# Kernel tuning notes

Measured on AMD Instinct MI355X. Metric: run time of the kernel, lower is better.

The kernel has to match this reference:

```python
import jax, jax.numpy as jnp
import numpy as np
from functools import partial

H = 50  # hidden size hardcoded in the module


def _lstm_cell(x, h, c, W_ih, W_hh, b_ih, b_hh):
    # PyTorch LSTMCell math, gate order i, f, g, o
    gates = x @ W_ih.T + h @ W_hh.T + b_ih + b_hh  # [B, 4H]
    i, f, g, o = jnp.split(gates, 4, axis=-1)
    c_new = jax.nn.sigmoid(f) * c + jax.nn.sigmoid(i) * jnp.tanh(g)
    h_new = jax.nn.sigmoid(o) * jnp.tanh(c_new)
    return h_new, c_new


def setup_inputs() -> dict:
    key = jax.random.key(0)
    ks = jax.random.split(key, 11)
    B, T = 512, 1024

    def w(k, shape, fan_in):
        return (jax.random.normal(k, shape, jnp.float32) / np.sqrt(fan_in)).astype(jnp.float32)

    return {
        "x": jax.random.normal(ks[0], (B, T), jnp.float32),
        "W_ih1": w(ks[1], (4 * H, 1), H),
        "W_hh1": w(ks[2], (4 * H, H), H),
        "b_ih1": w(ks[3], (4 * H,), H),
        "b_hh1": w(ks[4], (4 * H,), H),
        "W_ih2": w(ks[5], (4 * H, H), H),
        "W_hh2": w(ks[6], (4 * H, H), H),
        "b_ih2": w(ks[7], (4 * H,), H),
        "b_hh2": w(ks[8], (4 * H,), H),
        "W_lin": w(ks[9], (1, H), H),
        "b_lin": w(ks[10], (1,), H),
        "predict": 32,
    }


def reference(x, W_ih1, W_hh1, b_ih1, b_hh1, W_ih2, W_hh2, b_ih2, b_hh2,
              W_lin, b_lin, predict):
    B = x.shape[0]
    z = jnp.zeros((B, H), x.dtype)
    init = (z, z, z, z)

    def step(carry, x_t):  # x_t: [B, 1]
        h1, c1, h2, c2 = carry
        h1, c1 = _lstm_cell(x_t, h1, c1, W_ih1, W_hh1, b_ih1, b_hh1)
        h2, c2 = _lstm_cell(h1, h2, c2, W_ih2, W_hh2, b_ih2, b_hh2)
        out = h2 @ W_lin.T + b_lin  # [B, 1]
        return (h1, c1, h2, c2), out

    xs = jnp.swapaxes(x, 0, 1)[:, :, None]  # [T, B, 1]
    carry, outs = jax.lax.scan(step, init, xs)  # outs: [T, B, 1]

    if predict > 0:
        h1, c1, h2, c2 = carry

        def pstep(pcarry, _):
            h1, c1, h2, c2, o = pcarry
            h1, c1 = _lstm_cell(o, h1, c1, W_ih1, W_hh1, b_ih1, b_hh1)
            h2, c2 = _lstm_cell(h1, h2, c2, W_ih2, W_hh2, b_ih2, b_hh2)
            out = h2 @ W_lin.T + b_lin
            return (h1, c1, h2, c2, out), out

        _, pouts = jax.lax.scan(pstep, (h1, c1, h2, c2, outs[-1]), None, length=predict)
        outs = jnp.concatenate([outs, pouts], axis=0)

    # stack(dim=1).squeeze(2) -> [B, T + predict]
    return jnp.swapaxes(outs[..., 0], 0, 1)
```

## Files before the change

kernel.cpp:

```cpp
#include <hip/hip_runtime.h>


#define Hh   50
#define TLEN 1024

typedef _Float16 half2v __attribute__((ext_vector_type(2)));

#if __has_builtin(__builtin_amdgcn_fdot2)
#define FDOT2(a, b, c) __builtin_amdgcn_fdot2((a), (b), (c), false)
#else
#define FDOT2(a, b, c) ((c) + (float)(a)[0] * (float)(b)[0] + (float)(a)[1] * (float)(b)[1])
#endif

#define BC(f) __builtin_bit_cast(half2v, f)

#define DOT25(A0, A1, A2, A3, BASE, H) do {                                  \
    _Pragma("unroll")                                                        \
    for (int pq = 0; pq < 6; ++pq) {                                         \
        A0 = FDOT2(wgt[(BASE) + 4*pq + 0], BC(H[4*pq + 0]), A0);             \
        A1 = FDOT2(wgt[(BASE) + 4*pq + 1], BC(H[4*pq + 1]), A1);             \
        A2 = FDOT2(wgt[(BASE) + 4*pq + 2], BC(H[4*pq + 2]), A2);             \
        A3 = FDOT2(wgt[(BASE) + 4*pq + 3], BC(H[4*pq + 3]), A3);             \
    }                                                                        \
    A0 = FDOT2(wgt[(BASE) + 24], BC(H[24]), A0);                             \
} while (0)

__device__ __forceinline__ float fast_sigmoid(float v) {
    return 1.0f / (1.0f + __expf(-v));
}
__device__ __forceinline__ float fast_tanh(float v) {
    return 1.0f - 2.0f / (__expf(2.0f * v) + 1.0f);
}

extern "C" __global__ __launch_bounds__(256, 2)
void sine_lstm_kernel(const float* __restrict__ x,
                      const float* __restrict__ W_ih1,
                      const float* __restrict__ W_hh1,
                      const float* __restrict__ b_ih1,
                      const float* __restrict__ b_hh1,
                      const float* __restrict__ W_ih2,
                      const float* __restrict__ W_hh2,
                      const float* __restrict__ b_ih2,
                      const float* __restrict__ b_hh2,
                      const float* __restrict__ W_lin,
                      const float* __restrict__ b_lin,
                      const int*   __restrict__ predict_p,
                      float* __restrict__ out,
                      int T)
{
    __shared__ __align__(16) float    x_lds[TLEN];
    __shared__ __align__(16) _Float16 h1lds[2][64];
    __shared__ __align__(16) _Float16 h2lds[2][64];
    __shared__ __align__(16) float    h2f32[2][64];

    const int tid = threadIdx.x;
    const int wv  = tid >> 6;
    const int ln  = tid & 63;
    const bool isProd = (wv < 2);
    const int b   = blockIdx.x;
    const int predict = *predict_p;
    const int S = T + predict;

    for (int i = tid; i < TLEN; i += 256)
        x_lds[i] = x[(size_t)b * T + i];
    if (tid < 128) {
        ((_Float16*)h1lds)[tid] = (_Float16)0.0f;
        ((_Float16*)h2lds)[tid] = (_Float16)0.0f;
        ((float*)h2f32)[tid] = 0.0f;
    }

    const int  m    = (wv & 1) * 32 + (ln >> 1);
    const int  sub  = ln & 1;
    const bool mval = (m < Hh);
    const bool owner = mval && (sub == 0);
    const int  mc   = mval ? m : 0;
    const int  rowP = sub ? (Hh + mc)  : mc;
    const int  rowQ = sub ? (150 + mc) : (100 + mc);

    const float* MA = isProd ? W_hh1 : W_ih2;
    const float* MB = isProd ? W_hh1 : W_hh2;
    half2v wgt[100];
    #pragma unroll
    for (int p = 0; p < 25; ++p) {
        const int k0 = 2 * p, k1 = 2 * p + 1;
        wgt[p]      = half2v{(_Float16)MA[rowP * Hh + k0], (_Float16)MA[rowP * Hh + k1]};
        wgt[25 + p] = half2v{(_Float16)MA[rowQ * Hh + k0], (_Float16)MA[rowQ * Hh + k1]};
        wgt[50 + p] = half2v{(_Float16)MB[rowP * Hh + k0], (_Float16)MB[rowP * Hh + k1]};
        wgt[75 + p] = half2v{(_Float16)MB[rowQ * Hh + k0], (_Float16)MB[rowQ * Hh + k1]};
    }
    const float bP = isProd ? (b_ih1[rowP] + b_hh1[rowP]) : (b_ih2[rowP] + b_hh2[rowP]);
    const float bQ = isProd ? (b_ih1[rowQ] + b_hh1[rowQ]) : (b_ih2[rowQ] + b_hh2[rowQ]);
    const float wihP = W_ih1[rowP], wihQ = W_ih1[rowQ];
    const float wlin_l = (ln < Hh) ? W_lin[ln] : 0.0f;
    const float blin   = b_lin[0];

    float h1r[25], h2r[25];
    #pragma unroll
    for (int p = 0; p < 25; ++p) { h1r[p] = 0.0f; h2r[p] = 0.0f; }
    float cst = 0.0f;

    __syncthreads();

    for (int t = 0; t <= S; ++t) {
        __syncthreads();
        {
            const int s1 = (t + 1) & 1;
            #pragma unroll
            for (int L = 0; L < 6; ++L) {
                float4 f = *(const float4*)&h1lds[s1][8 * L];
                h1r[4*L] = f.x; h1r[4*L+1] = f.y; h1r[4*L+2] = f.z; h1r[4*L+3] = f.w;
            }
            h1r[24] = *(const float*)&h1lds[s1][48];
            const int s2 = t & 1;
            #pragma unroll
            for (int L = 0; L < 6; ++L) {
                float4 f = *(const float4*)&h2lds[s2][8 * L];
                h2r[4*L] = f.x; h2r[4*L+1] = f.y; h2r[4*L+2] = f.z; h2r[4*L+3] = f.w;
            }
            h2r[24] = *(const float*)&h2lds[s2][48];
        }
        const bool pred = (t >= T);

        if (!isProd && t >= 1) {
            float p0 = bP, p1 = 0.0f, p2 = 0.0f, p3 = 0.0f;
            float q0 = bQ, q1 = 0.0f, q2 = 0.0f, q3 = 0.0f;
            DOT25(p0, p1, p2, p3, 0,  h1r);
            DOT25(p0, p1, p2, p3, 50, h2r);
            DOT25(q0, q1, q2, q3, 25, h1r);
            DOT25(q0, q1, q2, q3, 75, h2r);
            float gP = (p0 + p2) + (p1 + p3);
            float gQ = (q0 + q2) + (q1 + q3);
            float eP = __shfl_xor(gP, 1);
            float eQ = __shfl_xor(gQ, 1);
            if (owner) {
                float cn = fast_sigmoid(eP) * cst + fast_sigmoid(gP) * fast_tanh(gQ);
                cst = cn;
                float hn = fast_sigmoid(eQ) * fast_tanh(cn);
                h2lds[(t + 1) & 1][m] = (_Float16)hn;
                h2f32[(t + 1) & 1][m] = hn;
            }
        }

        if (wv == 0 && t >= 2 && t <= T) {
            float part = (ln < Hh) ? h2f32[t & 1][ln] * wlin_l : 0.0f;
            #pragma unroll
            for (int off = 32; off > 0; off >>= 1)
                part += __shfl_down(part, off);
            if (ln == 0) out[(size_t)b * S + (t - 2)] = part + blin;
        }

        if (!pred) {
            if (isProd) {
                float xin = x_lds[t];
                float p0 = bP + xin * wihP, p1 = 0.0f, p2 = 0.0f, p3 = 0.0f;
                float q0 = bQ + xin * wihQ, q1 = 0.0f, q2 = 0.0f, q3 = 0.0f;
                DOT25(p0, p1, p2, p3, 0,  h1r);
                DOT25(q0, q1, q2, q3, 25, h1r);
                float gP = (p0 + p2) + (p1 + p3);
                float gQ = (q0 + q2) + (q1 + q3);
                float eP = __shfl_xor(gP, 1);
                float eQ = __shfl_xor(gQ, 1);
                if (owner) {
                    float cn = fast_sigmoid(eP) * cst + fast_sigmoid(gP) * fast_tanh(gQ);
                    cst = cn;
                    h1lds[t & 1][m] = (_Float16)(fast_sigmoid(eQ) * fast_tanh(cn));
                }
            }
        } else {
            __syncthreads();
            float part = (ln < Hh) ? h2f32[(t + 1) & 1][ln] * wlin_l : 0.0f;
            #pragma unroll
            for (int off = 32; off > 0; off >>= 1)
                part += __shfl_down(part, off);
            float o = __shfl(part, 0) + blin;
            if (tid == 0) out[(size_t)b * S + (t - 1)] = o;
            if (isProd && t < S) {
                float p0 = bP + o * wihP, p1 = 0.0f, p2 = 0.0f, p3 = 0.0f;
                float q0 = bQ + o * wihQ, q1 = 0.0f, q2 = 0.0f, q3 = 0.0f;
                DOT25(p0, p1, p2, p3, 0,  h1r);
                DOT25(q0, q1, q2, q3, 25, h1r);
                float gP = (p0 + p2) + (p1 + p3);
                float gQ = (q0 + q2) + (q1 + q3);
                float eP = __shfl_xor(gP, 1);
                float eQ = __shfl_xor(gQ, 1);
                if (owner) {
                    float cn = fast_sigmoid(eP) * cst + fast_sigmoid(gP) * fast_tanh(gQ);
                    cst = cn;
                    h1lds[t & 1][m] = (_Float16)(fast_sigmoid(eQ) * fast_tanh(cn));
                }
            }
        }
    }
}

extern "C" void kernel_launch(void* const* d_in, const int* in_sizes, int n_in,
                              void* d_out, int out_size, void* d_ws, size_t ws_size,
                              hipStream_t stream) {
    const float* x      = (const float*)d_in[0];
    const float* W_ih1  = (const float*)d_in[1];
    const float* W_hh1  = (const float*)d_in[2];
    const float* b_ih1  = (const float*)d_in[3];
    const float* b_hh1  = (const float*)d_in[4];
    const float* W_ih2  = (const float*)d_in[5];
    const float* W_hh2  = (const float*)d_in[6];
    const float* b_ih2  = (const float*)d_in[7];
    const float* b_hh2  = (const float*)d_in[8];
    const float* W_lin  = (const float*)d_in[9];
    const float* b_lin  = (const float*)d_in[10];
    const int*   pred   = (const int*)d_in[11];
    float* out = (float*)d_out;

    const int B = 512;
    const int T = in_sizes[0] / B;

    dim3 grid(B), block(256);
    hipLaunchKernelGGL(sine_lstm_kernel, grid, block, 0, stream,
                       x, W_ih1, W_hh1, b_ih1, b_hh1,
                       W_ih2, W_hh2, b_ih2, b_hh2,
                       W_lin, b_lin, pred, out, T);
}
```

Baseline: 1.064 ms.

## Split gate rows across four lanes per hidden unit with 512-thread blocks

Doubles the block to 512 threads and assigns each lane a single gate row, so four lanes cooperate per hidden unit instead of two lanes each computing two rows. This halves the per-thread dot-product chain on each serial timestep and halves the weight registers per thread. In exchange it adds a third cross-lane shuffle per step, raises the wave count per block, and puts more pressure on per-CU occupancy. Producer waves also stop loading the unused h2 state.

```diff
diff --git a/kernel.cpp b/kernel.cpp
--- a/kernel.cpp
+++ b/kernel.cpp
@@ -14,15 +14,15 @@
 
 #define BC(f) __builtin_bit_cast(half2v, f)
 
-#define DOT25(A0, A1, A2, A3, BASE, H) do {                                  \
+#define DOT25(A0, A1, A2, A3, W, H) do {                                     \
     _Pragma("unroll")                                                        \
     for (int pq = 0; pq < 6; ++pq) {                                         \
-        A0 = FDOT2(wgt[(BASE) + 4*pq + 0], BC(H[4*pq + 0]), A0);             \
-        A1 = FDOT2(wgt[(BASE) + 4*pq + 1], BC(H[4*pq + 1]), A1);             \
-        A2 = FDOT2(wgt[(BASE) + 4*pq + 2], BC(H[4*pq + 2]), A2);             \
-        A3 = FDOT2(wgt[(BASE) + 4*pq + 3], BC(H[4*pq + 3]), A3);             \
+        A0 = FDOT2(W[4*pq + 0], BC(H[4*pq + 0]), A0);                        \
+        A1 = FDOT2(W[4*pq + 1], BC(H[4*pq + 1]), A1);                        \
+        A2 = FDOT2(W[4*pq + 2], BC(H[4*pq + 2]), A2);                        \
+        A3 = FDOT2(W[4*pq + 3], BC(H[4*pq + 3]), A3);                        \
     }                                                                        \
-    A0 = FDOT2(wgt[(BASE) + 24], BC(H[24]), A0);                             \
+    A0 = FDOT2(W[24], BC(H[24]), A0);                                        \
 } while (0)
 
 __device__ __forceinline__ float fast_sigmoid(float v) {
@@ -32,7 +32,7 @@
     return 1.0f - 2.0f / (__expf(2.0f * v) + 1.0f);
 }
 
-extern "C" __global__ __launch_bounds__(256, 2)
+extern "C" __global__ __launch_bounds__(512, 2)
 void sine_lstm_kernel(const float* __restrict__ x,
                       const float* __restrict__ W_ih1,
                       const float* __restrict__ W_hh1,
@@ -56,12 +56,12 @@
     const int tid = threadIdx.x;
     const int wv  = tid >> 6;
     const int ln  = tid & 63;
-    const bool isProd = (wv < 2);
+    const bool isProd = (wv < 4);
     const int b   = blockIdx.x;
     const int predict = *predict_p;
     const int S = T + predict;
 
-    for (int i = tid; i < TLEN; i += 256)
+    for (int i = tid; i < TLEN; i += 512)
         x_lds[i] = x[(size_t)b * T + i];
     if (tid < 128) {
         ((_Float16*)h1lds)[tid] = (_Float16)0.0f;
@@ -69,28 +69,23 @@
         ((float*)h2f32)[tid] = 0.0f;
     }
 
-    const int  m    = (wv & 1) * 32 + (ln >> 1);
-    const int  sub  = ln & 1;
+    const int  m    = ((wv & 3) << 4) + (ln >> 2);
+    const int  q    = ln & 3;
     const bool mval = (m < Hh);
-    const bool owner = mval && (sub == 0);
-    const int  mc   = mval ? m : 0;
-    const int  rowP = sub ? (Hh + mc)  : mc;
-    const int  rowQ = sub ? (150 + mc) : (100 + mc);
+    const bool lead = mval && (q == 0);
+    const int  rc   = mval ? (q * Hh + m) : 0;
 
     const float* MA = isProd ? W_hh1 : W_ih2;
     const float* MB = isProd ? W_hh1 : W_hh2;
-    half2v wgt[100];
+    half2v wA[25], wB[25];
     #pragma unroll
     for (int p = 0; p < 25; ++p) {
         const int k0 = 2 * p, k1 = 2 * p + 1;
-        wgt[p]      = half2v{(_Float16)MA[rowP * Hh + k0], (_Float16)MA[rowP * Hh + k1]};
-        wgt[25 + p] = half2v{(_Float16)MA[rowQ * Hh + k0], (_Float16)MA[rowQ * Hh + k1]};
-        wgt[50 + p] = half2v{(_Float16)MB[rowP * Hh + k0], (_Float16)MB[rowP * Hh + k1]};
-        wgt[75 + p] = half2v{(_Float16)MB[rowQ * Hh + k0], (_Float16)MB[rowQ * Hh + k1]};
+        wA[p] = half2v{(_Float16)MA[rc * Hh + k0], (_Float16)MA[rc * Hh + k1]};
+        wB[p] = half2v{(_Float16)MB[rc * Hh + k0], (_Float16)MB[rc * Hh + k1]};
     }
-    const float bP = isProd ? (b_ih1[rowP] + b_hh1[rowP]) : (b_ih2[rowP] + b_hh2[rowP]);
-    const float bQ = isProd ? (b_ih1[rowQ] + b_hh1[rowQ]) : (b_ih2[rowQ] + b_hh2[rowQ]);
-    const float wihP = W_ih1[rowP], wihQ = W_ih1[rowQ];
+    const float bR   = isProd ? (b_ih1[rc] + b_hh1[rc]) : (b_ih2[rc] + b_hh2[rc]);
+    const float wihR = W_ih1[rc];
     const float wlin_l = (ln < Hh) ? W_lin[ln] : 0.0f;
     const float blin   = b_lin[0];
 
@@ -111,6 +106,8 @@
                 h1r[4*L] = f.x; h1r[4*L+1] = f.y; h1r[4*L+2] = f.z; h1r[4*L+3] = f.w;
             }
             h1r[24] = *(const float*)&h1lds[s1][48];
+        }
+        if (!isProd) {
             const int s2 = t & 1;
             #pragma unroll
             for (int L = 0; L < 6; ++L) {
@@ -122,20 +119,17 @@
         const bool pred = (t >= T);
 
         if (!isProd && t >= 1) {
-            float p0 = bP, p1 = 0.0f, p2 = 0.0f, p3 = 0.0f;
-            float q0 = bQ, q1 = 0.0f, q2 = 0.0f, q3 = 0.0f;
-            DOT25(p0, p1, p2, p3, 0,  h1r);
-            DOT25(p0, p1, p2, p3, 50, h2r);
-            DOT25(q0, q1, q2, q3, 25, h1r);
-            DOT25(q0, q1, q2, q3, 75, h2r);
-            float gP = (p0 + p2) + (p1 + p3);
-            float gQ = (q0 + q2) + (q1 + q3);
-            float eP = __shfl_xor(gP, 1);
-            float eQ = __shfl_xor(gQ, 1);
-            if (owner) {
-                float cn = fast_sigmoid(eP) * cst + fast_sigmoid(gP) * fast_tanh(gQ);
+            float a0 = bR, a1 = 0.0f, a2 = 0.0f, a3 = 0.0f;
+            DOT25(a0, a1, a2, a3, wA, h1r);
+            DOT25(a0, a1, a2, a3, wB, h2r);
+            float g  = (a0 + a2) + (a1 + a3);
+            float v1 = __shfl_xor(g, 1);
+            float v2 = __shfl_xor(g, 2);
+            float v3 = __shfl_xor(g, 3);
+            if (lead) {
+                float cn = fast_sigmoid(v1) * cst + fast_sigmoid(g) * fast_tanh(v2);
                 cst = cn;
-                float hn = fast_sigmoid(eQ) * fast_tanh(cn);
+                float hn = fast_sigmoid(v3) * fast_tanh(cn);
                 h2lds[(t + 1) & 1][m] = (_Float16)hn;
                 h2f32[(t + 1) & 1][m] = hn;
             }
@@ -152,18 +146,16 @@
         if (!pred) {
             if (isProd) {
                 float xin = x_lds[t];
-                float p0 = bP + xin * wihP, p1 = 0.0f, p2 = 0.0f, p3 = 0.0f;
-                float q0 = bQ + xin * wihQ, q1 = 0.0f, q2 = 0.0f, q3 = 0.0f;
-                DOT25(p0, p1, p2, p3, 0,  h1r);
-                DOT25(q0, q1, q2, q3, 25, h1r);
-                float gP = (p0 + p2) + (p1 + p3);
-                float gQ = (q0 + q2) + (q1 + q3);
-                float eP = __shfl_xor(gP, 1);
-                float eQ = __shfl_xor(gQ, 1);
-                if (owner) {
-                    float cn = fast_sigmoid(eP) * cst + fast_sigmoid(gP) * fast_tanh(gQ);
+                float a0 = bR + xin * wihR, a1 = 0.0f, a2 = 0.0f, a3 = 0.0f;
+                DOT25(a0, a1, a2, a3, wA, h1r);
+                float g  = (a0 + a2) + (a1 + a3);
+                float v1 = __shfl_xor(g, 1);
+                float v2 = __shfl_xor(g, 2);
+                float v3 = __shfl_xor(g, 3);
+                if (lead) {
+                    float cn = fast_sigmoid(v1) * cst + fast_sigmoid(g) * fast_tanh(v2);
                     cst = cn;
-                    h1lds[t & 1][m] = (_Float16)(fast_sigmoid(eQ) * fast_tanh(cn));
+                    h1lds[t & 1][m] = (_Float16)(fast_sigmoid(v3) * fast_tanh(cn));
                 }
             }
         } else {
@@ -175,18 +167,16 @@
             float o = __shfl(part, 0) + blin;
             if (tid == 0) out[(size_t)b * S + (t - 1)] = o;
             if (isProd && t < S) {
-                float p0 = bP + o * wihP, p1 = 0.0f, p2 = 0.0f, p3 = 0.0f;
-                float q0 = bQ + o * wihQ, q1 = 0.0f, q2 = 0.0f, q3 = 0.0f;
-                DOT25(p0, p1, p2, p3, 0,  h1r);
-                DOT25(q0, q1, q2, q3, 25, h1r);
-                float gP = (p0 + p2) + (p1 + p3);
-                float gQ = (q0 + q2) + (q1 + q3);
-                float eP = __shfl_xor(gP, 1);
-                float eQ = __shfl_xor(gQ, 1);
-                if (owner) {
-                    float cn = fast_sigmoid(eP) * cst + fast_sigmoid(gP) * fast_tanh(gQ);
+                float a0 = bR + o * wihR, a1 = 0.0f, a2 = 0.0f, a3 = 0.0f;
+                DOT25(a0, a1, a2, a3, wA, h1r);
+                float g  = (a0 + a2) + (a1 + a3);
+                float v1 = __shfl_xor(g, 1);
+                float v2 = __shfl_xor(g, 2);
+                float v3 = __shfl_xor(g, 3);
+                if (lead) {
+                    float cn = fast_sigmoid(v1) * cst + fast_sigmoid(g) * fast_tanh(v2);
                     cst = cn;
-                    h1lds[t & 1][m] = (_Float16)(fast_sigmoid(eQ) * fast_tanh(cn));
+                    h1lds[t & 1][m] = (_Float16)(fast_sigmoid(v3) * fast_tanh(cn));
                 }
             }
         }
@@ -213,7 +203,7 @@
     const int B = 512;
     const int T = in_sizes[0] / B;
 
-    dim3 grid(B), block(256);
+    dim3 grid(B), block(512);
     hipLaunchKernelGGL(sine_lstm_kernel, grid, block, 0, stream,
                        x, W_ih1, W_hh1, b_ih1, b_hh1,
                        W_ih2, W_hh2, b_ih2, b_hh2,
```

Measured after the change: 1.859 ms. +74.6%, slower.
